# Kernel tuning notes

Measured on AMD Instinct MI355X. Metric: run time of the kernel, lower is better.

## Reference

```python
import jax, jax.numpy as jnp
import numpy as np

D = 256      # linear_dim
H = 8        # heads
B, S = 4, 2048


def setup_inputs() -> dict:
    key = jax.random.key(0)
    ks = jax.random.split(key, 9)
    scale = 1.0 / np.sqrt(D)
    x = jax.random.normal(ks[0], (B, S, D), dtype=jnp.float32)
    # per-head Linear weights stacked: [H, out, in] (torch Linear layout)
    Wq = jax.random.normal(ks[1], (H, D, D), dtype=jnp.float32) * scale
    bq = jax.random.normal(ks[2], (H, D), dtype=jnp.float32) * scale
    Wk = jax.random.normal(ks[3], (H, D, D), dtype=jnp.float32) * scale
    bk = jax.random.normal(ks[4], (H, D), dtype=jnp.float32) * scale
    Wv = jax.random.normal(ks[5], (H, D, D), dtype=jnp.float32) * scale
    bv = jax.random.normal(ks[6], (H, D), dtype=jnp.float32) * scale
    Wo = jax.random.normal(ks[7], (D, H * D), dtype=jnp.float32) * (1.0 / np.sqrt(H * D))
    bo = jax.random.normal(ks[8], (D,), dtype=jnp.float32) * scale
    return {"x": x, "Wq": Wq, "bq": bq, "Wk": Wk, "bk": bk,
            "Wv": Wv, "bv": bv, "Wo": Wo, "bo": bo}


def reference(x, Wq, bq, Wk, bk, Wv, bv, Wo, bo):
    # Batched per-head projections (torch Linear: y = x @ W.T + b)
    Q = jnp.einsum('bsd,hed->bhse', x, Wq) + bq[None, :, None, :]  # [B,H,S,D]
    K = jnp.einsum('bsd,hed->bhse', x, Wk) + bk[None, :, None, :]
    V = jnp.einsum('bsd,hed->bhse', x, Wv) + bv[None, :, None, :]
    scores = jnp.einsum('bhse,bhte->bhst', Q, K) / jnp.sqrt(jnp.float32(D))  # [B,H,Sq,Sk]
    # FAITHFUL quirk: original softmaxes over dim=1 of [B,S,S] -> the QUERY axis.
    attn = jax.nn.softmax(scores, axis=2)
    Z = jnp.einsum('bhst,bhte->bhse', attn, V)       # [B,H,S,D]
    Z = jnp.transpose(Z, (0, 2, 1, 3)).reshape(B, S, H * D)  # concat heads (head-major order matches torch.cat)
    return jnp.einsum('bsf,of->bso', Z, Wo) + bo
```

## Files before the change

### kernel.cpp

```cpp
#include <hip/hip_runtime.h>
#include <hip/hip_bf16.h>

#define DEV __device__ __forceinline__

typedef __bf16 bf16x8 __attribute__((ext_vector_type(8)));
typedef float f32x4 __attribute__((ext_vector_type(4)));

DEV f32x4 mfma16(bf16x8 a, bf16x8 b, f32x4 c) {
  return __builtin_amdgcn_mfma_f32_16x16x32_bf16(a, b, c, 0, 0, 0);
}

DEV ushort f2bf(float f) {
  union { __hip_bfloat16 h; ushort u; } cv;
  cv.h = __float2bfloat16(f);
  return cv.u;
}
DEV float bf2f(ushort u) {
  union { float f; unsigned v; } cv; cv.v = ((unsigned)u) << 16; return cv.f;
}


__global__ __launch_bounds__(256) void convert_all(
    const float* __restrict__ x, const float* __restrict__ wq,
    const float* __restrict__ wk, const float* __restrict__ wv,
    const float* __restrict__ wo, ushort* __restrict__ dst)
{
  size_t i = ((size_t)blockIdx.x * 256 + threadIdx.x) * 4;
  const float* src; size_t off;
  if (i < (size_t)2097152) { src = x; off = i; }
  else {
    size_t j = i - 2097152;
    unsigned wsel = (unsigned)(j >> 19);
    off = j & 524287;
    src = wsel == 0 ? wq : wsel == 1 ? wk : wsel == 2 ? wv : wo;
  }
  float4 v = *(const float4*)(src + off);
  ushort4 o;
  o.x = f2bf(v.x); o.y = f2bf(v.y); o.z = f2bf(v.z); o.w = f2bf(v.w);
  *(ushort4*)(dst + i) = o;
}

template<int BM, int BN>
__global__ __launch_bounds__(256, 2) void gemm_qkv(
    const ushort* __restrict__ A,
    const ushort* __restrict__ W0, const ushort* __restrict__ W1, const ushort* __restrict__ W2,
    int K,
    const float* __restrict__ b0, const float* __restrict__ b1, const float* __restrict__ b2,
    ushort* __restrict__ Qo, ushort* __restrict__ Ko, ushort* __restrict__ Vo)
{
  constexpr int WM = BM / 2, WN = BN / 2, MF = WM / 16, NF = WN / 16;
  constexpr int CA = BM / 64, CB = BN / 64;
  const int n0 = blockIdx.x * BN, m0 = blockIdx.y * BM;
  const int tid = threadIdx.x, lane = tid & 63;
  const int wm = (tid >> 7) & 1, wn = (tid >> 6) & 1;

  __shared__ ushort As[BM * 40];
  __shared__ ushort Bs[BN * 40];

  const int p = n0 >> 11;
  const ushort* Bt = (p == 0 ? W0 : p == 1 ? W1 : W2) + (size_t)(n0 & 2047) * K;

  f32x4 acc[MF][NF];
#pragma unroll
  for (int m = 0; m < MF; m++)
#pragma unroll
    for (int n = 0; n < NF; n++) acc[m][n] = (f32x4){0.f, 0.f, 0.f, 0.f};

  for (int k0 = 0; k0 < K; k0 += 32) {
#pragma unroll
    for (int i = 0; i < CA; i++) {
      int ci = tid * CA + i; int r = ci >> 2, c = ci & 3;
      *(uint4*)&As[r * 40 + c * 8] = *(const uint4*)&A[(size_t)(m0 + r) * K + k0 + c * 8];
    }
#pragma unroll
    for (int i = 0; i < CB; i++) {
      int ci = tid * CB + i; int r = ci >> 2, c = ci & 3;
      *(uint4*)&Bs[r * 40 + c * 8] = *(const uint4*)&Bt[(size_t)r * K + k0 + c * 8];
    }
    __syncthreads();
    bf16x8 af[MF], bfr[NF];
#pragma unroll
    for (int m = 0; m < MF; m++)
      af[m] = *(const bf16x8*)&As[(wm * WM + m * 16 + (lane & 15)) * 40 + ((lane >> 4) << 3)];
#pragma unroll
    for (int n = 0; n < NF; n++)
      bfr[n] = *(const bf16x8*)&Bs[(wn * WN + n * 16 + (lane & 15)) * 40 + ((lane >> 4) << 3)];
#pragma unroll
    for (int m = 0; m < MF; m++)
#pragma unroll
      for (int n = 0; n < NF; n++) acc[m][n] = mfma16(af[m], bfr[n], acc[m][n]);
    __syncthreads();
  }

  const float* bias = (p == 0 ? b0 : p == 1 ? b1 : b2);
  const float scl = (p == 0 ? 0.0625f : 1.0f);
#pragma unroll
  for (int m = 0; m < MF; m++)
#pragma unroll
    for (int n = 0; n < NF; n++)
#pragma unroll
      for (int r = 0; r < 4; r++) {
        int row = m0 + wm * WM + m * 16 + ((lane >> 4) << 2) + r;
        int col = n0 + wn * WN + n * 16 + (lane & 15);
        int ce = col & 2047;
        float v = (acc[m][n][r] + bias[ce]) * scl;
        int b = row >> 11, s = row & 2047, h = ce >> 8, e = ce & 255;
        int bh = b * 8 + h;
        if (p == 0) {
          Qo[((size_t)(bh * 2048 + s) << 8) + e] = f2bf(v);
        } else if (p == 1) {
          int ee = ((((e >> 3) ^ (s & 7)) & 31) << 3) | (e & 7);
          Ko[((size_t)(bh * 2048 + s) << 8) + ee] = f2bf(v);
        } else {
          Vo[(((size_t)bh * 64 + (s >> 5)) << 13) + e * 32 + (s & 31)] = f2bf(v);
        }
      }
}

__global__ __launch_bounds__(256, 2) void gemm_out(
    const ushort* __restrict__ A, const ushort* __restrict__ Bw,
    const float* __restrict__ bias, float* __restrict__ out)
{
  const int n0 = blockIdx.x * 64, m0 = blockIdx.y * 64;
  const int tid = threadIdx.x, lane = tid & 63;
  const int wm = (tid >> 7) & 1, wn = (tid >> 6) & 1;
  const int g = lane >> 4, r15 = lane & 15;

  __shared__ ushort As[64 * 72];
  __shared__ ushort Bs[64 * 72];

  f32x4 acc[2][2];
#pragma unroll
  for (int m = 0; m < 2; m++)
#pragma unroll
    for (int n = 0; n < 2; n++) acc[m][n] = (f32x4){0.f, 0.f, 0.f, 0.f};

  for (int k0 = 0; k0 < 2048; k0 += 64) {
#pragma unroll
    for (int i = 0; i < 2; ++i) {
      int ci = tid * 2 + i, r = ci >> 3, c = ci & 7;
      *(uint4*)&As[r * 72 + c * 8] = *(const uint4*)&A[(size_t)(m0 + r) * 2048 + k0 + c * 8];
      *(uint4*)&Bs[r * 72 + c * 8] = *(const uint4*)&Bw[(size_t)(n0 + r) * 2048 + k0 + c * 8];
    }
    __syncthreads();
    bf16x8 af[2][2], bfr[2][2];
#pragma unroll
    for (int m = 0; m < 2; ++m)
#pragma unroll
      for (int k2 = 0; k2 < 2; ++k2)
        af[m][k2] = *(const bf16x8*)&As[(wm * 32 + m * 16 + r15) * 72 + k2 * 32 + g * 8];
#pragma unroll
    for (int n = 0; n < 2; ++n)
#pragma unroll
      for (int k2 = 0; k2 < 2; ++k2)
        bfr[n][k2] = *(const bf16x8*)&Bs[(wn * 32 + n * 16 + r15) * 72 + k2 * 32 + g * 8];
#pragma unroll
    for (int k2 = 0; k2 < 2; ++k2)
#pragma unroll
      for (int m = 0; m < 2; ++m)
#pragma unroll
        for (int n = 0; n < 2; ++n)
          acc[m][n] = mfma16(af[m][k2], bfr[n][k2], acc[m][n]);
    __syncthreads();
  }

#pragma unroll
  for (int m = 0; m < 2; m++)
#pragma unroll
    for (int n = 0; n < 2; n++)
#pragma unroll
      for (int r = 0; r < 4; r++) {
        int row = m0 + wm * 32 + m * 16 + g * 4 + r;
        int col = n0 + wn * 32 + n * 16 + r15;
        out[(size_t)row * 256 + col] = acc[m][n][r] + bias[col];
      }
}

__global__ __launch_bounds__(256, 4) void attn_p0(
    const ushort* __restrict__ Qb, const ushort* __restrict__ Kb,
    float* __restrict__ lpart)
{
  const int bid = blockIdx.x;
  const int swz = (bid & 7) * 128 + (bid >> 3);
  const int bh = swz >> 5, stile = swz & 31;
  const int s0 = stile * 64;
  const int tid = threadIdx.x, lane = tid & 63, w = tid >> 6;
  const int g = lane >> 4, r15 = lane & 15;

  __shared__ ushort Ks[2][8192];

  bf16x8 q[8];
  {
    const ushort* qrow = &Qb[((size_t)bh * 2048 + s0 + w * 16 + r15) * 256 + g * 8];
#pragma unroll
    for (int kk = 0; kk < 8; kk++) q[kk] = *(const bf16x8*)&qrow[kk * 32];
  }

  const ushort* Ktile = Kb + ((size_t)bh << 19);

  uint4 st[4];
#pragma unroll
  for (int i = 0; i < 4; ++i)
    st[i] = *(const uint4*)&Ktile[(size_t)(i * 256 + tid) * 8];
#pragma unroll
  for (int i = 0; i < 4; ++i)
    *(uint4*)&Ks[0][(i * 256 + tid) * 8] = st[i];

  int cur = 0;
  for (int it = 0; it < 64; ++it) {
    __syncthreads();
    if (it < 63) {
#pragma unroll
      for (int i = 0; i < 4; ++i)
        st[i] = *(const uint4*)&Ktile[(size_t)(it + 1) * 8192 + (i * 256 + tid) * 8];
    }
    f32x4 gg[2];
    gg[0] = (f32x4){0.f, 0.f, 0.f, 0.f};
    gg[1] = (f32x4){0.f, 0.f, 0.f, 0.f};
    const ushort* ks = &Ks[cur][0];
#pragma unroll
    for (int n = 0; n < 2; ++n)
#pragma unroll
      for (int kk = 0; kk < 8; ++kk) {
        bf16x8 kb = *(const bf16x8*)&ks[(n * 16 + r15) * 256 + (((kk * 4 + g) ^ (r15 & 7)) << 3)];
        gg[n] = mfma16(q[kk], kb, gg[n]);
      }
#pragma unroll
    for (int n = 0; n < 2; ++n) {
      float sn = __expf(gg[n][0]) + __expf(gg[n][1]) + __expf(gg[n][2]) + __expf(gg[n][3]);
      sn += __shfl_xor(sn, 16);
      sn += __shfl_xor(sn, 32);
      if (g == 0)
        lpart[((size_t)((stile * 4 + w) * 32 + bh) << 11) + it * 32 + n * 16 + r15] = sn;
    }
    if (it < 63) {
#pragma unroll
      for (int i = 0; i < 4; ++i)
        *(uint4*)&Ks[cur ^ 1][(i * 256 + tid) * 8] = st[i];
    }
    cur ^= 1;
  }
}

__global__ __launch_bounds__(256, 2) void attn_p1(
    const ushort* __restrict__ Qb, const ushort* __restrict__ Kb,
    const ushort* __restrict__ Vt, ushort* __restrict__ Zb)
{
  const int bid = blockIdx.x;
  const int swz = (bid & 7) * 64 + (bid >> 3);
  const int bh = swz >> 4, stile = swz & 15;
  const int s0 = stile * 128;
  const int tid = threadIdx.x, lane = tid & 63, w = tid >> 6;
  const int g = lane >> 4, r15 = lane & 15;

  __shared__ __align__(16) ushort Ks[2][8192];
  __shared__ __align__(16) ushort Ps[2][5120];

  bf16x8 q[2][8];
#pragma unroll
  for (int h = 0; h < 2; ++h) {
    const ushort* qrow = &Qb[((size_t)bh * 2048 + s0 + w * 32 + h * 16 + r15) * 256 + g * 8];
#pragma unroll
    for (int kk = 0; kk < 8; kk++) q[h][kk] = *(const bf16x8*)&qrow[kk * 32];
  }

  const ushort* Ktile = Kb + ((size_t)bh << 19);
  const ushort* Vtile = Vt + ((size_t)bh << 19);

  f32x4 acc[8][4];
#pragma unroll
  for (int m = 0; m < 8; m++)
#pragma unroll
    for (int n = 0; n < 4; n++) acc[m][n] = (f32x4){0.f, 0.f, 0.f, 0.f};

  {
    uint4 p0[4];
#pragma unroll
    for (int i = 0; i < 4; ++i)
      p0[i] = *(const uint4*)&Ktile[(size_t)(i * 256 + tid) * 8];
#pragma unroll
    for (int i = 0; i < 4; ++i)
      *(uint4*)&Ks[0][(i * 256 + tid) * 8] = p0[i];
  }
  __syncthreads();

  for (int it = 0; it < 64; ++it) {
    const int cur = it & 1;
    bf16x8 vb[4];
#pragma unroll
    for (int n = 0; n < 4; ++n)
      vb[n] = *(const bf16x8*)&Vtile[(size_t)it * 8192 + (w * 64 + n * 16 + r15) * 32 + g * 8];
    uint4 st[4];
    if (it < 63) {
#pragma unroll
      for (int i = 0; i < 4; ++i)
        st[i] = *(const uint4*)&Ktile[(size_t)(it + 1) * 8192 + (i * 256 + tid) * 8];
    }

#pragma unroll
    for (int h = 0; h < 2; ++h) {
      f32x4 gg[2];
      gg[0] = (f32x4){0.f, 0.f, 0.f, 0.f};
      gg[1] = (f32x4){0.f, 0.f, 0.f, 0.f};
#pragma unroll
      for (int n = 0; n < 2; ++n)
#pragma unroll
        for (int kk = 0; kk < 8; ++kk) {
          bf16x8 kb = *(const bf16x8*)&Ks[cur][(n * 16 + r15) * 256 + (((kk * 4 + g) ^ (r15 & 7)) << 3)];
          gg[n] = mfma16(q[h][kk], kb, gg[n]);
        }
#pragma unroll
      for (int n = 0; n < 2; ++n)
#pragma unroll
        for (int rr = 0; rr < 4; ++rr)
          Ps[cur][(w * 32 + h * 16 + g * 4 + rr) * 40 + n * 16 + r15] = f2bf(__expf(gg[n][rr]));
    }

    if (it < 63) {
#pragma unroll
      for (int i = 0; i < 4; ++i)
        *(uint4*)&Ks[cur ^ 1][(i * 256 + tid) * 8] = st[i];
    }

    __syncthreads();

#pragma unroll
    for (int mh = 0; mh < 2; ++mh) {
      bf16x8 pa[4];
#pragma unroll
      for (int m = 0; m < 4; ++m)
        pa[m] = *(const bf16x8*)&Ps[cur][((mh * 4 + m) * 16 + r15) * 40 + g * 8];
#pragma unroll
      for (int n = 0; n < 4; ++n)
#pragma unroll
        for (int m = 0; m < 4; ++m)
          acc[mh * 4 + m][n] = mfma16(pa[m], vb[n], acc[mh * 4 + m][n]);
    }
  }

  const int b = bh >> 3, h = bh & 7;
#pragma unroll
  for (int m = 0; m < 8; m++)
#pragma unroll
    for (int n = 0; n < 4; n++)
#pragma unroll
      for (int rr = 0; rr < 4; rr++) {
        int sl = m * 16 + g * 4 + rr;
        int el = w * 64 + n * 16 + r15;
        Zb[((size_t)(b * 2048 + s0 + sl)) * 2048 + h * 256 + el] = f2bf(acc[m][n][rr]);
      }
}

__global__ __launch_bounds__(256) void vscale(
    ushort* __restrict__ Vt, const float* __restrict__ lp)
{
  const int tt = blockIdx.x, bh = blockIdx.y, tid = threadIdx.x;
  const int t = tid & 31, pg = tid >> 5;
  __shared__ float red[256];
  __shared__ float cinv[32];
  float s = 0.f;
  for (int p = pg * 16; p < pg * 16 + 16; ++p)
    s += lp[(((size_t)p * 32 + bh) << 11) + tt * 32 + t];
  red[tid] = s;
  __syncthreads();
  if (tid < 32) {
    float tot = 0.f;
#pragma unroll
    for (int i = 0; i < 8; ++i) tot += red[tid + i * 32];
    cinv[tid] = 1.0f / tot;
  }
  __syncthreads();
  size_t base = (((size_t)bh * 64 + tt) << 13) + (size_t)tid * 32;
  ushort buf[32];
#pragma unroll
  for (int i = 0; i < 4; ++i) *(uint4*)&buf[i * 8] = *(const uint4*)&Vt[base + i * 8];
#pragma unroll
  for (int j = 0; j < 32; ++j) buf[j] = f2bf(bf2f(buf[j]) * cinv[j]);
#pragma unroll
  for (int i = 0; i < 4; ++i) *(uint4*)&Vt[base + i * 8] = *(const uint4*)&buf[i * 8];
}

extern "C" void kernel_launch(void* const* d_in, const int* in_sizes, int n_in,
                              void* d_out, int out_size, void* d_ws, size_t ws_size,
                              hipStream_t stream) {
  const float* x  = (const float*)d_in[0];
  const float* Wq = (const float*)d_in[1];
  const float* bq = (const float*)d_in[2];
  const float* Wk = (const float*)d_in[3];
  const float* bk = (const float*)d_in[4];
  const float* Wv = (const float*)d_in[5];
  const float* bv = (const float*)d_in[6];
  const float* Wo = (const float*)d_in[7];
  const float* bo = (const float*)d_in[8];

  if (ws_size < (size_t)176160768) return;

  char* ws = (char*)d_ws;
  ushort* bfb = (ushort*)ws;
  ushort* xb  = bfb;
  ushort* wqb = bfb + 2097152;
  ushort* wkb = bfb + 2621440;
  ushort* wvb = bfb + 3145728;
  ushort* wob = bfb + 3670016;
  ushort* Qb = (ushort*)(ws + 8388608);
  ushort* Kb = (ushort*)(ws + 41943040);
  ushort* Vt = (ushort*)(ws + 75497472);
  ushort* Zb = (ushort*)(ws + 109051904);
  float*  lp = (float*)(ws + 142606336);
  float* out = (float*)d_out;

  convert_all<<<4096, 256, 0, stream>>>(x, Wq, Wk, Wv, Wo, bfb);
  gemm_qkv<128, 128><<<dim3(48, 64), 256, 0, stream>>>(
      xb, wqb, wkb, wvb, 256, bq, bk, bv, Qb, Kb, Vt);
  attn_p0<<<1024, 256, 0, stream>>>(Qb, Kb, lp);
  vscale<<<dim3(64, 32), 256, 0, stream>>>(Vt, lp);
  attn_p1<<<512, 256, 0, stream>>>(Qb, Kb, Vt, Zb);
  gemm_out<<<dim3(4, 128), 256, 0, stream>>>(Zb, wob, bo, out);
}
```

Measured before the change: 377.9 us.

## Widen attn_p0 query tile to 128 rows and split key range across blocks

attn_p0 now gives each block 128 query rows (two 16-row groups per wave) and half of the key tiles, so every K tile staged in LDS feeds twice as many MFMAs and the 16 KB K tile is read from global half as often. The double-buffered prefetch is replaced by a single buffer with load-then-sync, and Q fragments are pinned in registers through an asm barrier. attn_p1's QK loop is reordered so each K fragment read from LDS serves both query halves. vscale's partial-sum count drops to match the new lpart layout. The cost is higher register pressure and lost overlap between global loads and compute in attn_p0.

After: 347.0 us. 1.09x faster.

```diff
diff --git a/kernel.cpp b/kernel.cpp
--- a/kernel.cpp
+++ b/kernel.cpp
@@ -182,63 +182,58 @@
 {
   const int bid = blockIdx.x;
   const int swz = (bid & 7) * 128 + (bid >> 3);
-  const int bh = swz >> 5, stile = swz & 31;
-  const int s0 = stile * 64;
+  const int bh = swz >> 5, stile = (swz >> 1) & 15, half = swz & 1;
+  const int s0 = stile * 128;
   const int tid = threadIdx.x, lane = tid & 63, w = tid >> 6;
   const int g = lane >> 4, r15 = lane & 15;
 
-  __shared__ ushort Ks[2][8192];
-
-  bf16x8 q[8];
-  {
-    const ushort* qrow = &Qb[((size_t)bh * 2048 + s0 + w * 16 + r15) * 256 + g * 8];
-#pragma unroll
-    for (int kk = 0; kk < 8; kk++) q[kk] = *(const bf16x8*)&qrow[kk * 32];
-  }
+  __shared__ __align__(16) ushort Ks[8192];
+
+  uint4 qr[2][8];
+#pragma unroll
+  for (int h = 0; h < 2; ++h) {
+    const ushort* qrow = &Qb[((size_t)bh * 2048 + s0 + w * 32 + h * 16 + r15) * 256 + g * 8];
+#pragma unroll
+    for (int kk = 0; kk < 8; kk++) qr[h][kk] = *(const uint4*)&qrow[kk * 32];
+  }
+#pragma unroll
+  for (int h = 0; h < 2; ++h)
+#pragma unroll
+    for (int kk = 0; kk < 8; kk++)
+      asm volatile("" : "+v"(qr[h][kk].x), "+v"(qr[h][kk].y),
+                        "+v"(qr[h][kk].z), "+v"(qr[h][kk].w));
 
   const ushort* Ktile = Kb + ((size_t)bh << 19);
-
-  uint4 st[4];
-#pragma unroll
-  for (int i = 0; i < 4; ++i)
-    st[i] = *(const uint4*)&Ktile[(size_t)(i * 256 + tid) * 8];
-#pragma unroll
-  for (int i = 0; i < 4; ++i)
-    *(uint4*)&Ks[0][(i * 256 + tid) * 8] = st[i];
-
-  int cur = 0;
-  for (int it = 0; it < 64; ++it) {
-    __syncthreads();
-    if (it < 63) {
-#pragma unroll
-      for (int i = 0; i < 4; ++i)
-        st[i] = *(const uint4*)&Ktile[(size_t)(it + 1) * 8192 + (i * 256 + tid) * 8];
-    }
-    f32x4 gg[2];
-    gg[0] = (f32x4){0.f, 0.f, 0.f, 0.f};
-    gg[1] = (f32x4){0.f, 0.f, 0.f, 0.f};
-    const ushort* ks = &Ks[cur][0];
-#pragma unroll
-    for (int n = 0; n < 2; ++n)
+  const int it0 = half * 32, it1 = it0 + 32;
+
+  for (int it = it0; it < it1; ++it) {
+    uint4 st[4];
+#pragma unroll
+    for (int i = 0; i < 4; ++i)
+      st[i] = *(const uint4*)&Ktile[(size_t)it * 8192 + (i * 256 + tid) * 8];
+#pragma unroll
+    for (int i = 0; i < 4; ++i)
+      *(uint4*)&Ks[(i * 256 + tid) * 8] = st[i];
+    __syncthreads();
+
+#pragma unroll
+    for (int n = 0; n < 2; ++n) {
+      f32x4 g0 = (f32x4){0.f, 0.f, 0.f, 0.f};
+      f32x4 g1 = (f32x4){0.f, 0.f, 0.f, 0.f};
 #pragma unroll
       for (int kk = 0; kk < 8; ++kk) {
-        bf16x8 kb = *(const bf16x8*)&ks[(n * 16 + r15) * 256 + (((kk * 4 + g) ^ (r15 & 7)) << 3)];
-        gg[n] = mfma16(q[kk], kb, gg[n]);
-      }
-#pragma unroll
-    for (int n = 0; n < 2; ++n) {
-      float sn = __expf(gg[n][0]) + __expf(gg[n][1]) + __expf(gg[n][2]) + __expf(gg[n][3]);
+        bf16x8 kb = *(const bf16x8*)&Ks[(n * 16 + r15) * 256 + (((kk * 4 + g) ^ (r15 & 7)) << 3)];
+        g0 = mfma16(*(const bf16x8*)&qr[0][kk], kb, g0);
+        g1 = mfma16(*(const bf16x8*)&qr[1][kk], kb, g1);
+      }
+      float sn = __expf(g0[0]) + __expf(g0[1]) + __expf(g0[2]) + __expf(g0[3])
+               + __expf(g1[0]) + __expf(g1[1]) + __expf(g1[2]) + __expf(g1[3]);
       sn += __shfl_xor(sn, 16);
       sn += __shfl_xor(sn, 32);
       if (g == 0)
         lpart[((size_t)((stile * 4 + w) * 32 + bh) << 11) + it * 32 + n * 16 + r15] = sn;
     }
-    if (it < 63) {
-#pragma unroll
-      for (int i = 0; i < 4; ++i)
-        *(uint4*)&Ks[cur ^ 1][(i * 256 + tid) * 8] = st[i];
-    }
-    cur ^= 1;
+    __syncthreads();
   }
 }
 
@@ -298,22 +293,20 @@
     }
 
 #pragma unroll
-    for (int h = 0; h < 2; ++h) {
-      f32x4 gg[2];
-      gg[0] = (f32x4){0.f, 0.f, 0.f, 0.f};
-      gg[1] = (f32x4){0.f, 0.f, 0.f, 0.f};
-#pragma unroll
-      for (int n = 0; n < 2; ++n)
-#pragma unroll
-        for (int kk = 0; kk < 8; ++kk) {
-          bf16x8 kb = *(const bf16x8*)&Ks[cur][(n * 16 + r15) * 256 + (((kk * 4 + g) ^ (r15 & 7)) << 3)];
-          gg[n] = mfma16(q[h][kk], kb, gg[n]);
-        }
-#pragma unroll
-      for (int n = 0; n < 2; ++n)
-#pragma unroll
-        for (int rr = 0; rr < 4; ++rr)
-          Ps[cur][(w * 32 + h * 16 + g * 4 + rr) * 40 + n * 16 + r15] = f2bf(__expf(gg[n][rr]));
+    for (int n = 0; n < 2; ++n) {
+      f32x4 g0 = (f32x4){0.f, 0.f, 0.f, 0.f};
+      f32x4 g1 = (f32x4){0.f, 0.f, 0.f, 0.f};
+#pragma unroll
+      for (int kk = 0; kk < 8; ++kk) {
+        bf16x8 kb = *(const bf16x8*)&Ks[cur][(n * 16 + r15) * 256 + (((kk * 4 + g) ^ (r15 & 7)) << 3)];
+        g0 = mfma16(q[0][kk], kb, g0);
+        g1 = mfma16(q[1][kk], kb, g1);
+      }
+#pragma unroll
+      for (int rr = 0; rr < 4; ++rr) {
+        Ps[cur][(w * 32 + g * 4 + rr) * 40 + n * 16 + r15] = f2bf(__expf(g0[rr]));
+        Ps[cur][(w * 32 + 16 + g * 4 + rr) * 40 + n * 16 + r15] = f2bf(__expf(g1[rr]));
+      }
     }
 
     if (it < 63) {
@@ -359,7 +352,7 @@
   __shared__ float red[256];
   __shared__ float cinv[32];
   float s = 0.f;
-  for (int p = pg * 16; p < pg * 16 + 16; ++p)
+  for (int p = pg * 8; p < pg * 8 + 8; ++p)
     s += lp[(((size_t)p * 32 + bh) << 11) + tt * 32 + t];
   red[tid] = s;
   __syncthreads();
```
